# Kernel optimization log

Hardware: AMD Instinct MI355X
Metric: run time of the kernel (lower is better)

The kernel has to match this reference:

```python
import jax, jax.numpy as jnp
import numpy as np

B, T, C, N = 4, 2048, 1024, 16
D = C // N


def setup_inputs() -> dict:
    key = jax.random.key(0)
    ks = jax.random.split(key, 10)
    s = 1.0 / np.sqrt(C)
    x = jax.random.normal(ks[0], (B, T, C), dtype=jnp.float32)
    token_mask = jax.random.randint(ks[1], (B, T), 0, 2, dtype=jnp.int32)
    token_mask = token_mask.at[:, 0].set(1)  # keep col 0 valid so no all--inf row
    inp = {"x": x, "token_mask": token_mask}
    for i, name in enumerate(["q", "k", "v", "p"]):
        inp[f"w{name}"] = jax.random.uniform(ks[2 + 2 * i], (C, C), jnp.float32, -s, s)
        inp[f"b{name}"] = jax.random.uniform(ks[3 + 2 * i], (C,), jnp.float32, -s, s)
    return inp


def reference(x, token_mask, wq, bq, wk, bk, wv, bv, wp, bp):
    # projections: nn.Linear computes x @ W.T + b
    q = (x @ wq.T + bq).reshape(B, T, N, D)
    k = (x @ wk.T + bk).reshape(B, T, N, D)
    v = (x @ wv.T + bv).reshape(B, T, N, D)
    # scores: (B, N, T, T)
    scores = jnp.einsum("bqnd,bknd->bnqk", q, k) / jnp.sqrt(jnp.float32(D))
    causal = jnp.tril(jnp.ones((T, T), dtype=bool))
    valid = causal[None, None] & (token_mask[:, None, None, :] != 0)
    scores = jnp.where(valid, scores, -jnp.inf)
    probs = jax.nn.softmax(scores, axis=-1)
    attn = jnp.einsum("bnqk,bknd->bqnd", probs, v).reshape(B, T, C)
    out = attn @ wp.T + bp
    return out
```

## Files before the change

kernel.cpp:

```cpp
#include <hip/hip_runtime.h>
#include <hip/hip_bf16.h>
#include <math.h>

typedef short bf16x8 __attribute__((ext_vector_type(8)));
typedef float f32x4 __attribute__((ext_vector_type(4)));

#if __has_builtin(__builtin_amdgcn_exp2f)
#define EXP2F(x) __builtin_amdgcn_exp2f(x)
#else
#define EXP2F(x) __expf(0.69314718056f * (x))
#endif

__device__ __forceinline__ unsigned short f2bf(float f) {
    union { float f; unsigned u; } v; v.f = f;
    unsigned r = v.u + 0x7fffu + ((v.u >> 16) & 1u);
    return (unsigned short)(r >> 16);
}

__device__ __forceinline__ unsigned pack_bf2(float a, float b) {
    __hip_bfloat162 h = __float22bfloat162_rn(float2{a, b});
    union { __hip_bfloat162 h; unsigned u; } c; c.h = h;
    return c.u;
}

__device__ __forceinline__ void gld_lds16(const unsigned short* g, const unsigned short* l) {
    __builtin_amdgcn_global_load_lds(
        (const __attribute__((address_space(1))) void*)g,
        (__attribute__((address_space(3))) void*)l, 16, 0, 0);
}

__global__ void cvt_f32_bf16(const float* __restrict__ src, unsigned short* __restrict__ dst, int n) {
    int i = (blockIdx.x * blockDim.x + threadIdx.x) * 4;
    if (i < n) {
        float4 f = *(const float4*)(src + i);
        ushort4 o;
        o.x = f2bf(f.x); o.y = f2bf(f.y); o.z = f2bf(f.z); o.w = f2bf(f.w);
        *(ushort4*)(dst + i) = o;
    }
}

__global__ void cvt4_f32_bf16(const float* s0, const float* s1, const float* s2, const float* s3,
                              unsigned short* d0, unsigned short* d1, unsigned short* d2,
                              unsigned short* d3, int n) {
    const float* s; unsigned short* d;
    switch (blockIdx.y) {
        case 0: s = s0; d = d0; break;
        case 1: s = s1; d = d1; break;
        case 2: s = s2; d = d2; break;
        default: s = s3; d = d3; break;
    }
    int i = (blockIdx.x * blockDim.x + threadIdx.x) * 4;
    if (i < n) {
        float4 f = *(const float4*)(s + i);
        ushort4 o;
        o.x = f2bf(f.x); o.y = f2bf(f.y); o.z = f2bf(f.z); o.w = f2bf(f.w);
        *(ushort4*)(d + i) = o;
    }
}

__global__ void mask_to_f(const int* __restrict__ tm, float* __restrict__ ma, int n) {
    int i = blockIdx.x * blockDim.x + threadIdx.x;
    if (i < n) ma[i] = tm[i] ? 0.0f : -__builtin_inff();
}

__global__ __launch_bounds__(256, 4) void gemm_bt(
        const unsigned short* __restrict__ A, const unsigned short* __restrict__ W,
        const float* __restrict__ b0p, const float* __restrict__ b1p,
        const float* __restrict__ b2p, float* __restrict__ outF,
        unsigned short* __restrict__ outB, unsigned short* __restrict__ vt,
        int M, int Nlog, int K) {
    __shared__ __align__(16) unsigned short As[2][128][32];
    __shared__ __align__(16) unsigned short Ws[2][128][32];
    const size_t BUFS = (size_t)8192 * 1024;
    const int m0 = blockIdx.y * 128, n0 = blockIdx.x * 128;
    const int tid = threadIdx.x, lane = tid & 63, w = tid >> 6;
    const int quad = lane >> 4, lc = lane & 15;
    const int wr = (w >> 1) * 64, wc = (w & 1) * 64;
    const int sr = lane >> 2, sc = (lane & 3) * 8;

    const int buf = n0 >> 10;
    const float* bias = buf == 0 ? b0p : (buf == 1 ? b1p : b2p);

    auto stage = [&](int s, int k0) {
        gld_lds16(A + (size_t)(m0 + w * 32 +      sr) * K + k0 + sc, &As[s][w * 32     ][0]);
        gld_lds16(A + (size_t)(m0 + w * 32 + 16 + sr) * K + k0 + sc, &As[s][w * 32 + 16][0]);
        gld_lds16(W + (size_t)(n0 + w * 32 +      sr) * K + k0 + sc, &Ws[s][w * 32     ][0]);
        gld_lds16(W + (size_t)(n0 + w * 32 + 16 + sr) * K + k0 + sc, &Ws[s][w * 32 + 16][0]);
    };

    f32x4 acc[4][4] = {};
    stage(0, 0);

    for (int k0 = 0; k0 < K; k0 += 32) {
        const int cur = (k0 >> 5) & 1;
        __syncthreads();
        if (k0 + 32 < K) stage(cur ^ 1, k0 + 32);
        bf16x8 af[4], bw[4];
        #pragma unroll
        for (int i = 0; i < 4; ++i) af[i] = *(const bf16x8*)&As[cur][wr + i * 16 + lc][quad * 8];
        #pragma unroll
        for (int j = 0; j < 4; ++j) bw[j] = *(const bf16x8*)&Ws[cur][wc + j * 16 + lc][quad * 8];
        #pragma unroll
        for (int i = 0; i < 4; ++i)
            #pragma unroll
            for (int j = 0; j < 4; ++j)
                acc[i][j] = __builtin_amdgcn_mfma_f32_16x16x32_bf16(af[i], bw[j], acc[i][j], 0, 0, 0);
    }

    #pragma unroll
    for (int j = 0; j < 4; ++j) {
        int col = n0 + wc + j * 16 + lc;
        int coll = col & 1023;
        float bj = bias[coll];
        #pragma unroll
        for (int i = 0; i < 4; ++i) {
            int rowb = m0 + wr + i * 16 + quad * 4;
            if (buf == 2) {
                int bb = rowb >> 11, t = rowb & 2047;
                int hh = coll >> 6, dd = coll & 63;
                ushort4 o4;
                o4.x = f2bf(acc[i][j][0] + bj);
                o4.y = f2bf(acc[i][j][1] + bj);
                o4.z = f2bf(acc[i][j][2] + bj);
                o4.w = f2bf(acc[i][j][3] + bj);
                *(ushort4*)(vt + ((size_t)(bb * 16 + hh) * 64 + dd) * 2048 + t) = o4;
            } else {
                #pragma unroll
                for (int r = 0; r < 4; ++r) {
                    float v = acc[i][j][r] + bj;
                    size_t idx = (size_t)buf * BUFS + (size_t)(rowb + r) * 1024 + coll;
                    if (outB) outB[idx] = f2bf(v);
                    else      outF[idx] = v;
                }
            }
        }
    }
}

__global__ __launch_bounds__(256, 4) void attn_kernel(
        const unsigned short* __restrict__ Q, const unsigned short* __restrict__ K,
        const unsigned short* __restrict__ Vt, const float* __restrict__ maskadd,
        unsigned short* __restrict__ O) {
    const int T = 2048, C = 1024;
    __shared__ __align__(16) unsigned short Kl[64][64];
    __shared__ __align__(16) unsigned short Vl[2][64][64];
    __shared__ __align__(16) unsigned short Pl[4][16][72];

    const int pair = blockIdx.x;
    const int bn = blockIdx.y;
    const int b = bn >> 4, h = bn & 15;
    const int tid = threadIdx.x, w = tid >> 6, lane = tid & 63;
    const int quad = lane >> 4, lc = lane & 15;
    const float NEG_INF = -__builtin_inff();
    const float CSC = 0.18033688011112042f;

    const unsigned short* Kbh = K + (size_t)b * T * C + h * 64;
    const unsigned short* Vbh = Vt + (size_t)(b * 16 + h) * 64 * 2048;

    const int lrow = lane >> 3;
    const int swz8 = ((lane & 7) ^ (lrow & 7)) * 8;
    const int kb0 = (quad ^ (lc & 7)) * 8;

    auto stageK = [&](int kt) {
        #pragma unroll
        for (int ch = 0; ch < 2; ++ch)
            gld_lds16(Kbh + (size_t)(kt * 64 + w * 16 + ch * 8 + lrow) * C + swz8,
                      &Kl[w * 16 + ch * 8][0]);
    };
    auto stageV = [&](int kt, int s) {
        #pragma unroll
        for (int ch = 0; ch < 2; ++ch)
            gld_lds16(Vbh + (size_t)(w * 16 + ch * 8 + lrow) * 2048 + kt * 64 + swz8,
                      &Vl[s][w * 16 + ch * 8][0]);
    };

    #pragma unroll 1
    for (int half = 0; half < 2; ++half) {
        const int qt = half ? (31 - pair) : pair;

        if (half) __syncthreads();
        stageK(0);
        stageV(0, 0);

        size_t qrow = (size_t)(b * T + qt * 64 + w * 16 + lc) * C + h * 64;
        bf16x8 qb0 = *(const bf16x8*)(Q + qrow + quad * 8);
        bf16x8 qb1 = *(const bf16x8*)(Q + qrow + 32 + quad * 8);

        f32x4 oaccT[4] = {};
        float m = NEG_INF, l = 0.f;
        const int qg = qt * 64 + w * 16 + lc;

        #pragma unroll 1
        for (int kt = 0; kt <= qt; ++kt) {
            const int slot = kt & 1;
            __syncthreads();

            f32x4 mk[4];
            #pragma unroll
            for (int j = 0; j < 4; ++j)
                mk[j] = *(const f32x4*)(maskadd + b * T + kt * 64 + j * 16 + quad * 4);

            f32x4 sacc[4] = {};
            #pragma unroll
            for (int j = 0; j < 4; ++j) {
                bf16x8 ka0 = *(const bf16x8*)&Kl[j * 16 + lc][kb0];
                bf16x8 ka1 = *(const bf16x8*)&Kl[j * 16 + lc][kb0 ^ 32];
                sacc[j] = __builtin_amdgcn_mfma_f32_16x16x32_bf16(ka0, qb0, sacc[j], 0, 0, 0);
                sacc[j] = __builtin_amdgcn_mfma_f32_16x16x32_bf16(ka1, qb1, sacc[j], 0, 0, 0);
            }

            __syncthreads();
            if (kt < qt) {
                stageK(kt + 1);
                stageV(kt + 1, slot ^ 1);
            }

            float s[4][4];
            float mx = NEG_INF;
            #pragma unroll
            for (int j = 0; j < 4; ++j) {
                #pragma unroll
                for (int r = 0; r < 4; ++r) {
                    float sv = fmaf(sacc[j][r], CSC, mk[j][r]);
                    if (kt == qt) {
                        int kg = kt * 64 + j * 16 + quad * 4 + r;
                        if (kg > qg) sv = NEG_INF;
                    }
                    s[j][r] = sv;
                    mx = fmaxf(mx, sv);
                }
            }
            mx = fmaxf(mx, __shfl_xor(mx, 16, 64));
            mx = fmaxf(mx, __shfl_xor(mx, 32, 64));
            float mnew = fmaxf(m, mx);
            float alpha = EXP2F(m - mnew);
            m = mnew;
            float ps = 0.f;
            #pragma unroll
            for (int j = 0; j < 4; ++j)
                #pragma unroll
                for (int r = 0; r < 4; ++r) {
                    float p = EXP2F(s[j][r] - mnew);
                    s[j][r] = p;
                    ps += p;
                }
            ps += __shfl_xor(ps, 16, 64);
            ps += __shfl_xor(ps, 32, 64);
            l = l * alpha + ps;
            #pragma unroll
            for (int jd = 0; jd < 4; ++jd) oaccT[jd] *= alpha;

            #pragma unroll
            for (int j = 0; j < 4; ++j) {
                uint2 pk;
                pk.x = pack_bf2(s[j][0], s[j][1]);
                pk.y = pack_bf2(s[j][2], s[j][3]);
                *(uint2*)&Pl[w][lc][j * 16 + quad * 4] = pk;
            }
            bf16x8 pb0 = *(const bf16x8*)&Pl[w][lc][quad * 8];
            bf16x8 pb1 = *(const bf16x8*)&Pl[w][lc][32 + quad * 8];

            #pragma unroll
            for (int jd = 0; jd < 4; ++jd) {
                bf16x8 va0 = *(const bf16x8*)&Vl[slot][jd * 16 + lc][kb0];
                bf16x8 va1 = *(const bf16x8*)&Vl[slot][jd * 16 + lc][kb0 ^ 32];
                oaccT[jd] = __builtin_amdgcn_mfma_f32_16x16x32_bf16(va0, pb0, oaccT[jd], 0, 0, 0);
                oaccT[jd] = __builtin_amdgcn_mfma_f32_16x16x32_bf16(va1, pb1, oaccT[jd], 0, 0, 0);
            }
        }

        float inv = 1.0f / l;
        size_t orow = (size_t)(b * T + qt * 64 + w * 16 + lc) * C + h * 64;
        #pragma unroll
        for (int jd = 0; jd < 4; ++jd) {
            ushort4 o4;
            o4.x = f2bf(oaccT[jd][0] * inv);
            o4.y = f2bf(oaccT[jd][1] * inv);
            o4.z = f2bf(oaccT[jd][2] * inv);
            o4.w = f2bf(oaccT[jd][3] * inv);
            *(ushort4*)(O + orow + jd * 16 + quad * 4) = o4;
        }
    }
}

extern "C" void kernel_launch(void* const* d_in, const int* in_sizes, int n_in,
                              void* d_out, int out_size, void* d_ws, size_t ws_size,
                              hipStream_t stream) {
    const float* x  = (const float*)d_in[0];
    const int* tm   = (const int*)d_in[1];
    const float* wq = (const float*)d_in[2]; const float* bq = (const float*)d_in[3];
    const float* wk = (const float*)d_in[4]; const float* bk = (const float*)d_in[5];
    const float* wv = (const float*)d_in[6]; const float* bv = (const float*)d_in[7];
    const float* wp = (const float*)d_in[8]; const float* bp = (const float*)d_in[9];
    float* out = (float*)d_out;

    const int Bv = 4, Tv = 2048, Cv = 1024;
    const size_t MT = (size_t)Bv * Tv;
    const size_t XN = MT * Cv;
    const size_t WN = (size_t)Cv * Cv;

    unsigned short* xb  = (unsigned short*)d_ws;
    unsigned short* wqb = xb  + XN;
    unsigned short* wkb = wqb + WN;
    unsigned short* wvb = wkb + WN;
    unsigned short* wpb = wvb + WN;
    unsigned short* Qb  = wpb + WN;
    unsigned short* Kb  = Qb + XN;
    unsigned short* Vtb = Kb + XN;
    unsigned short* Ab  = xb;
    float* maskadd = (float*)d_out;

    cvt_f32_bf16<<<XN / 1024, 256, 0, stream>>>(x, xb, (int)XN);
    cvt4_f32_bf16<<<dim3(WN / 1024, 4), 256, 0, stream>>>(wq, wk, wv, wp, wqb, wkb, wvb, wpb, (int)WN);
    mask_to_f<<<(int)(MT / 256), 256, 0, stream>>>(tm, maskadd, (int)MT);

    gemm_bt<<<dim3(24, 64), 256, 0, stream>>>(xb, wqb, bq, bk, bv, nullptr, Qb, Vtb, (int)MT, 3072, Cv);

    attn_kernel<<<dim3(16, Bv * 16), 256, 0, stream>>>(Qb, Kb, Vtb, maskadd, Ab);

    gemm_bt<<<dim3(8, 64), 256, 0, stream>>>(Ab, wpb, bp, bp, bp, out, nullptr, nullptr, (int)MT, 1024, Cv);
}
```

Measured before the change: 303.6 us.

## Restructure attention to 128-row query blocks with 32x32 MFMA and register-resident P

The attention kernel now processes 128 query rows per block (32 per wave) using 32x32x16 bf16 MFMAs and double-buffers K as well as V, so only one barrier per key tile is needed. P is repacked in registers with v_permlane32_swap instead of a round trip through LDS. The online-softmax rescale is skipped unless the running max grows by more than a threshold, and the block index is swizzled so blocks of the same head are spread out. The aim is more work per K/V tile load, fewer LDS round trips and barriers, and denser matrix-core use, at the cost of more registers (launch bounds lowered to 2 blocks per CU) and coarser causal load balancing.

New measurement: 296.7 us. -2.3%, faster.

```diff
diff --git a/kernel.cpp b/kernel.cpp
--- a/kernel.cpp
+++ b/kernel.cpp
@@ -4,6 +4,7 @@
 
 typedef short bf16x8 __attribute__((ext_vector_type(8)));
 typedef float f32x4 __attribute__((ext_vector_type(4)));
+typedef float f32x16 __attribute__((ext_vector_type(16)));
 
 #if __has_builtin(__builtin_amdgcn_exp2f)
 #define EXP2F(x) __builtin_amdgcn_exp2f(x)
@@ -137,20 +138,22 @@
     }
 }
 
-__global__ __launch_bounds__(256, 4) void attn_kernel(
+__global__ __launch_bounds__(256, 2) void attn_kernel(
         const unsigned short* __restrict__ Q, const unsigned short* __restrict__ K,
         const unsigned short* __restrict__ Vt, const float* __restrict__ maskadd,
         unsigned short* __restrict__ O) {
     const int T = 2048, C = 1024;
-    __shared__ __align__(16) unsigned short Kl[64][64];
+    __shared__ __align__(16) unsigned short Kl[2][64][64];
     __shared__ __align__(16) unsigned short Vl[2][64][64];
-    __shared__ __align__(16) unsigned short Pl[4][16][72];
-
-    const int pair = blockIdx.x;
-    const int bn = blockIdx.y;
+
+    const int lid = blockIdx.y * 8 + blockIdx.x;
+    const int sw = (lid & 7) * 64 + (lid >> 3);
+    const int pair = sw & 7;
+    const int bn = sw >> 3;
     const int b = bn >> 4, h = bn & 15;
+
     const int tid = threadIdx.x, w = tid >> 6, lane = tid & 63;
-    const int quad = lane >> 4, lc = lane & 15;
+    const int lq = lane & 31, hi = lane >> 5;
     const float NEG_INF = -__builtin_inff();
     const float CSC = 0.18033688011112042f;
 
@@ -159,13 +162,13 @@
 
     const int lrow = lane >> 3;
     const int swz8 = ((lane & 7) ^ (lrow & 7)) * 8;
-    const int kb0 = (quad ^ (lc & 7)) * 8;
-
-    auto stageK = [&](int kt) {
+    const int rdsw = lq & 7;
+
+    auto stageK = [&](int kt, int s) {
         #pragma unroll
         for (int ch = 0; ch < 2; ++ch)
             gld_lds16(Kbh + (size_t)(kt * 64 + w * 16 + ch * 8 + lrow) * C + swz8,
-                      &Kl[w * 16 + ch * 8][0]);
+                      &Kl[s][w * 16 + ch * 8][0]);
     };
     auto stageV = [&](int kt, int s) {
         #pragma unroll
@@ -176,110 +179,130 @@
 
     #pragma unroll 1
     for (int half = 0; half < 2; ++half) {
-        const int qt = half ? (31 - pair) : pair;
+        const int qb = half ? (15 - pair) : pair;
+        const int qbase = qb * 128;
+        const int KT = 2 * qb + 2;
+        const int Q0 = qbase + w * 32;
+        const int ktd = Q0 >> 6;
+        const int qg = Q0 + lq;
 
         if (half) __syncthreads();
-        stageK(0);
+        stageK(0, 0);
         stageV(0, 0);
 
-        size_t qrow = (size_t)(b * T + qt * 64 + w * 16 + lc) * C + h * 64;
-        bf16x8 qb0 = *(const bf16x8*)(Q + qrow + quad * 8);
-        bf16x8 qb1 = *(const bf16x8*)(Q + qrow + 32 + quad * 8);
-
-        f32x4 oaccT[4] = {};
+        const unsigned short* Qp = Q + (size_t)(b * T + Q0 + lq) * C + h * 64 + hi * 8;
+        bf16x8 qf[4];
+        #pragma unroll
+        for (int i = 0; i < 4; ++i) qf[i] = *(const bf16x8*)(Qp + i * 16);
+
+        f32x16 oacc[2] = {};
         float m = NEG_INF, l = 0.f;
-        const int qg = qt * 64 + w * 16 + lc;
 
         #pragma unroll 1
-        for (int kt = 0; kt <= qt; ++kt) {
+        for (int kt = 0; kt < KT; ++kt) {
             const int slot = kt & 1;
             __syncthreads();
-
-            f32x4 mk[4];
-            #pragma unroll
-            for (int j = 0; j < 4; ++j)
-                mk[j] = *(const f32x4*)(maskadd + b * T + kt * 64 + j * 16 + quad * 4);
-
-            f32x4 sacc[4] = {};
-            #pragma unroll
-            for (int j = 0; j < 4; ++j) {
-                bf16x8 ka0 = *(const bf16x8*)&Kl[j * 16 + lc][kb0];
-                bf16x8 ka1 = *(const bf16x8*)&Kl[j * 16 + lc][kb0 ^ 32];
-                sacc[j] = __builtin_amdgcn_mfma_f32_16x16x32_bf16(ka0, qb0, sacc[j], 0, 0, 0);
-                sacc[j] = __builtin_amdgcn_mfma_f32_16x16x32_bf16(ka1, qb1, sacc[j], 0, 0, 0);
-            }
-
-            __syncthreads();
-            if (kt < qt) {
-                stageK(kt + 1);
+            if (kt + 1 < KT) {
+                stageK(kt + 1, slot ^ 1);
                 stageV(kt + 1, slot ^ 1);
             }
 
-            float s[4][4];
-            float mx = NEG_INF;
-            #pragma unroll
-            for (int j = 0; j < 4; ++j) {
-                #pragma unroll
-                for (int r = 0; r < 4; ++r) {
-                    float sv = fmaf(sacc[j][r], CSC, mk[j][r]);
-                    if (kt == qt) {
-                        int kg = kt * 64 + j * 16 + quad * 4 + r;
-                        if (kg > qg) sv = NEG_INF;
+            if (kt > ktd) continue;
+
+            f32x4 mkv[8];
+            const float* mb = maskadd + b * T + kt * 64 + hi * 4;
+            #pragma unroll
+            for (int g = 0; g < 8; ++g)
+                mkv[g] = *(const f32x4*)(mb + (g >> 2) * 32 + (g & 3) * 8);
+
+            f32x16 sacc[2] = {};
+            __builtin_amdgcn_s_setprio(1);
+            #pragma unroll
+            for (int kh = 0; kh < 2; ++kh)
+                #pragma unroll
+                for (int i = 0; i < 4; ++i) {
+                    bf16x8 kf = *(const bf16x8*)&Kl[slot][kh * 32 + lq][(((i << 1) | hi) ^ rdsw) * 8];
+                    sacc[kh] = __builtin_amdgcn_mfma_f32_32x32x16_bf16(kf, qf[i], sacc[kh], 0, 0, 0);
+                }
+            __builtin_amdgcn_s_setprio(0);
+
+            float tmax = NEG_INF;
+            const bool diag = (kt == ktd);
+            #pragma unroll
+            for (int kh = 0; kh < 2; ++kh)
+                #pragma unroll
+                for (int r = 0; r < 16; ++r) {
+                    float x = fmaf(sacc[kh][r], CSC, mkv[kh * 4 + (r >> 2)][r & 3]);
+                    if (diag) {
+                        int kg = kt * 64 + kh * 32 + (r >> 2) * 8 + hi * 4 + (r & 3);
+                        if (kg > qg) x = NEG_INF;
                     }
-                    s[j][r] = sv;
-                    mx = fmaxf(mx, sv);
-                }
-            }
-            mx = fmaxf(mx, __shfl_xor(mx, 16, 64));
-            mx = fmaxf(mx, __shfl_xor(mx, 32, 64));
-            float mnew = fmaxf(m, mx);
-            float alpha = EXP2F(m - mnew);
-            m = mnew;
+                    sacc[kh][r] = x;
+                    tmax = fmaxf(tmax, x);
+                }
+            tmax = fmaxf(tmax, __shfl_xor(tmax, 32, 64));
+
+            if (__any(tmax > m + 8.0f)) {
+                float mnew = fmaxf(m, tmax);
+                float al = EXP2F(m - mnew);
+                m = mnew; l *= al;
+                #pragma unroll
+                for (int dh = 0; dh < 2; ++dh)
+                    #pragma unroll
+                    for (int r = 0; r < 16; ++r) oacc[dh][r] *= al;
+            }
+
             float ps = 0.f;
             #pragma unroll
-            for (int j = 0; j < 4; ++j)
-                #pragma unroll
-                for (int r = 0; r < 4; ++r) {
-                    float p = EXP2F(s[j][r] - mnew);
-                    s[j][r] = p;
+            for (int kh = 0; kh < 2; ++kh)
+                #pragma unroll
+                for (int r = 0; r < 16; ++r) {
+                    float p = EXP2F(sacc[kh][r] - m);
+                    sacc[kh][r] = p;
                     ps += p;
                 }
-            ps += __shfl_xor(ps, 16, 64);
             ps += __shfl_xor(ps, 32, 64);
-            l = l * alpha + ps;
-            #pragma unroll
-            for (int jd = 0; jd < 4; ++jd) oaccT[jd] *= alpha;
-
-            #pragma unroll
-            for (int j = 0; j < 4; ++j) {
-                uint2 pk;
-                pk.x = pack_bf2(s[j][0], s[j][1]);
-                pk.y = pack_bf2(s[j][2], s[j][3]);
-                *(uint2*)&Pl[w][lc][j * 16 + quad * 4] = pk;
-            }
-            bf16x8 pb0 = *(const bf16x8*)&Pl[w][lc][quad * 8];
-            bf16x8 pb1 = *(const bf16x8*)&Pl[w][lc][32 + quad * 8];
-
-            #pragma unroll
-            for (int jd = 0; jd < 4; ++jd) {
-                bf16x8 va0 = *(const bf16x8*)&Vl[slot][jd * 16 + lc][kb0];
-                bf16x8 va1 = *(const bf16x8*)&Vl[slot][jd * 16 + lc][kb0 ^ 32];
-                oaccT[jd] = __builtin_amdgcn_mfma_f32_16x16x32_bf16(va0, pb0, oaccT[jd], 0, 0, 0);
-                oaccT[jd] = __builtin_amdgcn_mfma_f32_16x16x32_bf16(va1, pb1, oaccT[jd], 0, 0, 0);
-            }
+            l += ps;
+
+            bf16x8 pb[4];
+            #pragma unroll
+            for (int i = 0; i < 4; ++i) {
+                const int kh = i >> 1, ro = (i & 1) * 8;
+                unsigned pa = pack_bf2(sacc[kh][ro + 0], sacc[kh][ro + 1]);
+                unsigned pe = pack_bf2(sacc[kh][ro + 4], sacc[kh][ro + 5]);
+                unsigned pc = pack_bf2(sacc[kh][ro + 2], sacc[kh][ro + 3]);
+                unsigned pd = pack_bf2(sacc[kh][ro + 6], sacc[kh][ro + 7]);
+                asm("v_permlane32_swap_b32 %0, %1" : "+v"(pa), "+v"(pe));
+                asm("v_permlane32_swap_b32 %0, %1" : "+v"(pc), "+v"(pd));
+                union { unsigned u[4]; bf16x8 v; } uu;
+                uu.u[0] = pa; uu.u[1] = pc; uu.u[2] = pe; uu.u[3] = pd;
+                pb[i] = uu.v;
+            }
+
+            __builtin_amdgcn_s_setprio(1);
+            #pragma unroll
+            for (int dh = 0; dh < 2; ++dh)
+                #pragma unroll
+                for (int i = 0; i < 4; ++i) {
+                    bf16x8 vf = *(const bf16x8*)&Vl[slot][dh * 32 + lq][(((i << 1) | hi) ^ rdsw) * 8];
+                    oacc[dh] = __builtin_amdgcn_mfma_f32_32x32x16_bf16(vf, pb[i], oacc[dh], 0, 0, 0);
+                }
+            __builtin_amdgcn_s_setprio(0);
         }
 
         float inv = 1.0f / l;
-        size_t orow = (size_t)(b * T + qt * 64 + w * 16 + lc) * C + h * 64;
-        #pragma unroll
-        for (int jd = 0; jd < 4; ++jd) {
-            ushort4 o4;
-            o4.x = f2bf(oaccT[jd][0] * inv);
-            o4.y = f2bf(oaccT[jd][1] * inv);
-            o4.z = f2bf(oaccT[jd][2] * inv);
-            o4.w = f2bf(oaccT[jd][3] * inv);
-            *(ushort4*)(O + orow + jd * 16 + quad * 4) = o4;
-        }
+        size_t orow = (size_t)(b * T + Q0 + lq) * C + h * 64;
+        #pragma unroll
+        for (int dh = 0; dh < 2; ++dh)
+            #pragma unroll
+            for (int g = 0; g < 4; ++g) {
+                ushort4 o4;
+                o4.x = f2bf(oacc[dh][g * 4 + 0] * inv);
+                o4.y = f2bf(oacc[dh][g * 4 + 1] * inv);
+                o4.z = f2bf(oacc[dh][g * 4 + 2] * inv);
+                o4.w = f2bf(oacc[dh][g * 4 + 3] * inv);
+                *(ushort4*)(O + orow + dh * 32 + g * 8 + hi * 4) = o4;
+            }
     }
 }
 
@@ -316,7 +339,7 @@
 
     gemm_bt<<<dim3(24, 64), 256, 0, stream>>>(xb, wqb, bq, bk, bv, nullptr, Qb, Vtb, (int)MT, 3072, Cv);
 
-    attn_kernel<<<dim3(16, Bv * 16), 256, 0, stream>>>(Qb, Kb, Vtb, maskadd, Ab);
+    attn_kernel<<<dim3(8, Bv * 16), 256, 0, stream>>>(Qb, Kb, Vtb, maskadd, Ab);
 
     gemm_bt<<<dim3(8, 64), 256, 0, stream>>>(Ab, wpb, bp, bp, bp, out, nullptr, nullptr, (int)MT, 1024, Cv);
 }
```
